# Optimization experiments

Hardware: AMD Instinct MI355X
Metric: run time of the kernel (lower is better)

The kernel has to match this reference:

```python
import jax, jax.numpy as jnp
import numpy as np

INTERVAL = 4
Q = 2 ** INTERVAL          # 16, quantization step
L = 2 ** (8 - INTERVAL) + 1  # 17, LUT size per axis


def round_ste(x):
    # round in forward, identity in backward (BPDA)
    return x + jax.lax.stop_gradient(jnp.round(x) - x)


def setup_inputs() -> dict:
    key = jax.random.key(0)
    k1, k2, k3 = jax.random.split(key, 3)
    # pixel values in [0, 255)
    img = jax.random.uniform(k1, (2, 3, 1080, 1920), jnp.float32) * 255.0
    # int8 LUT / 127 -> values in [-1, 1], shape [L^3, 3, 1, 1]
    lut = jax.random.uniform(k2, (L ** 3, 3, 1, 1), jnp.float32, -1.0, 1.0)
    # color correction matrix, scaled so final output mostly lands in [0,1]
    ccm = (jnp.eye(3, dtype=jnp.float32) + 0.05 * jax.random.normal(k3, (3, 3), jnp.float32)) / 127.0
    return {"img": img, "lut": lut, "ccm": ccm}


def _lut3d_interp(img, lut):
    """Trilinear 3D-LUT interpolation (InterpTorch3DBatch). img: [B,3,H,W]."""
    B, C, H, W = img.shape
    # _prepare_3d_lut_weights: scale, round with STE, clamp
    w = jnp.clip(round_ste(lut * 127.0), -127.0, 127.0)[:, :, 0, 0]  # [L^3, 3]
    flat = img.transpose(0, 2, 3, 1).reshape(-1, 3)  # [N, 3] per-pixel rgb
    r, g, b = flat[:, 0], flat[:, 1], flat[:, 2]
    r1 = jnp.floor(r / Q).astype(jnp.int32)
    g1 = jnp.floor(g / Q).astype(jnp.int32)
    b1 = jnp.floor(b / Q).astype(jnp.int32)
    fr = jnp.mod(r, float(Q))
    fg = jnp.mod(g, float(Q))
    fb = jnp.mod(b, float(Q))
    r2 = jnp.clip(r1 + 1, 0, L - 1)
    g2 = jnp.clip(g1 + 1, 0, L - 1)
    b2 = jnp.clip(b1 + 1, 0, L - 1)

    def corner(i, j, k):
        return w[i * (L * L) + j * L + k]  # [N, 3] gather

    p000 = corner(r1, g1, b1); p001 = corner(r1, g1, b2)
    p010 = corner(r1, g2, b1); p011 = corner(r1, g2, b2)
    p100 = corner(r2, g1, b1); p101 = corner(r2, g1, b2)
    p110 = corner(r2, g2, b1); p111 = corner(r2, g2, b2)

    fr = (fr / Q)[:, None]; fg = (fg / Q)[:, None]; fb = (fb / Q)[:, None]
    c00 = p000 * (1 - fr) + p100 * fr
    c01 = p001 * (1 - fr) + p101 * fr
    c10 = p010 * (1 - fr) + p110 * fr
    c11 = p011 * (1 - fr) + p111 * fr
    c0 = c00 * (1 - fg) + c10 * fg
    c1 = c01 * (1 - fg) + c11 * fg
    out = c0 * (1 - fb) + c1 * fb  # [N, 3]
    return out, (B, H, W, C)


def reference(img, lut, ccm):
    out_pix, (B, H, W, C) = _lut3d_interp(img, lut)
    # apply_color: per-pixel 3x3 color matrix (tensordot dims [[-1],[-1]]) + clamp
    out_pix = jnp.clip(out_pix @ ccm.T, 1e-8, 1.0)
    return out_pix.reshape(B, H, W, C).transpose(0, 3, 1, 2)
```

## Files before the change

### kernel.cpp

```cpp
#include <hip/hip_runtime.h>
#include <cstdint>

#define LUT_L    17
#define LUT_LL   289
#define NLUT     4913
#define NLUT_PAD 4916
#define IMG_B    2
#define IMG_H    1080
#define IMG_W    1920
#define PLANE    (IMG_H * IMG_W)
#define NPIX     (IMG_B * PLANE)
#define NQUAD    (NPIX / 4)
#define QPB      1024
#define NFULL    (NQUAD / QPB)

typedef float nfloat4 __attribute__((ext_vector_type(4)));

__device__ __forceinline__ int pack_entry(const float* __restrict__ lut, int idx) {
    float r = lut[idx * 3 + 0] * 127.0f;
    float g = lut[idx * 3 + 1] * 127.0f;
    float b = lut[idx * 3 + 2] * 127.0f;
    int ir = (int)rintf(r);
    int ig = (int)rintf(g);
    int ib = (int)rintf(b);
    ir = max(-127, min(127, ir));
    ig = max(-127, min(127, ig));
    ib = max(-127, min(127, ib));
    return (ir & 0xff) | ((ig & 0xff) << 8) | ((ib & 0xff) << 16);
}

__global__ void pack_lut_kernel(const float* __restrict__ lut, int* __restrict__ wq) {
    int idx = blockIdx.x * blockDim.x + threadIdx.x;
    if (idx >= NLUT_PAD) return;
    wq[idx] = (idx < NLUT) ? pack_entry(lut, idx) : 0;
}

__device__ __forceinline__ float up0(int v) { return (float)((v << 24) >> 24); }
__device__ __forceinline__ float up1(int v) { return (float)((v << 16) >> 24); }
__device__ __forceinline__ float up2(int v) { return (float)((v <<  8) >> 24); }

__device__ __forceinline__ float clamp01eps(float x) {
    return fminf(fmaxf(x, 1e-8f), 1.0f);
}

__device__ __forceinline__ void px_process(float r, float g, float b,
                                           const int* wq,
                                           const float* __restrict__ m,
                                           float& o0, float& o1, float& o2) {
    float rq = r * 0.0625f, gq = g * 0.0625f, bq = b * 0.0625f;
    float rf = floorf(rq), gf = floorf(gq), bf = floorf(bq);
    float fr = rq - rf, fg = gq - gf, fb = bq - bf;
    int i1 = (int)rf, j1 = (int)gf, k1 = (int)bf;

    const int* r00 = wq + (i1 * LUT_LL + j1 * LUT_L + k1);
    const int* r01 = r00 + LUT_L;
    const int* r10 = r00 + LUT_LL;
    const int* r11 = r10 + LUT_L;
    int w000 = r00[0], w001 = r00[1];
    int w010 = r01[0], w011 = r01[1];
    int w100 = r10[0], w101 = r10[1];
    int w110 = r11[0], w111 = r11[1];

    float wr0 = 1.0f - fr, wg0 = 1.0f - fg, wb0 = 1.0f - fb;
    float a00 = wg0 * wb0, a01 = wg0 * fb, a10 = fg * wb0, a11 = fg * fb;
    float s000 = wr0 * a00, s001 = wr0 * a01, s010 = wr0 * a10, s011 = wr0 * a11;
    float s100 = fr  * a00, s101 = fr  * a01, s110 = fr  * a10, s111 = fr  * a11;

    float pr = s000 * up0(w000);
    pr = fmaf(s001, up0(w001), pr); pr = fmaf(s010, up0(w010), pr);
    pr = fmaf(s011, up0(w011), pr); pr = fmaf(s100, up0(w100), pr);
    pr = fmaf(s101, up0(w101), pr); pr = fmaf(s110, up0(w110), pr);
    pr = fmaf(s111, up0(w111), pr);

    float pg = s000 * up1(w000);
    pg = fmaf(s001, up1(w001), pg); pg = fmaf(s010, up1(w010), pg);
    pg = fmaf(s011, up1(w011), pg); pg = fmaf(s100, up1(w100), pg);
    pg = fmaf(s101, up1(w101), pg); pg = fmaf(s110, up1(w110), pg);
    pg = fmaf(s111, up1(w111), pg);

    float pb = s000 * up2(w000);
    pb = fmaf(s001, up2(w001), pb); pb = fmaf(s010, up2(w010), pb);
    pb = fmaf(s011, up2(w011), pb); pb = fmaf(s100, up2(w100), pb);
    pb = fmaf(s101, up2(w101), pb); pb = fmaf(s110, up2(w110), pb);
    pb = fmaf(s111, up2(w111), pb);

    o0 = clamp01eps(fmaf(pr, m[0], fmaf(pg, m[1], pb * m[2])));
    o1 = clamp01eps(fmaf(pr, m[3], fmaf(pg, m[4], pb * m[5])));
    o2 = clamp01eps(fmaf(pr, m[6], fmaf(pg, m[7], pb * m[8])));
}

__device__ __forceinline__ void do_quad(const float* __restrict__ img,
                                        float* __restrict__ out,
                                        const int* wq, const float* __restrict__ m,
                                        int q) {
    int p = q * 4;
    int bimg = p / PLANE;
    int hw = p - bimg * PLANE;
    size_t base = (size_t)bimg * 3 * PLANE + hw;

    nfloat4 R  = *(const nfloat4*)(img + base);
    nfloat4 G  = *(const nfloat4*)(img + base + PLANE);
    nfloat4 Bv = *(const nfloat4*)(img + base + 2 * PLANE);

    float o0x, o0y, o0z, o0w;
    float o1x, o1y, o1z, o1w;
    float o2x, o2y, o2z, o2w;

    px_process(R.x, G.x, Bv.x, wq, m, o0x, o1x, o2x);
    px_process(R.y, G.y, Bv.y, wq, m, o0y, o1y, o2y);
    px_process(R.z, G.z, Bv.z, wq, m, o0z, o1z, o2z);
    px_process(R.w, G.w, Bv.w, wq, m, o0w, o1w, o2w);

    nfloat4 O0 = {o0x, o0y, o0z, o0w};
    nfloat4 O1 = {o1x, o1y, o1z, o1w};
    nfloat4 O2 = {o2x, o2y, o2z, o2w};

    __builtin_nontemporal_store(O0, (nfloat4*)(out + base));
    __builtin_nontemporal_store(O1, (nfloat4*)(out + base + PLANE));
    __builtin_nontemporal_store(O2, (nfloat4*)(out + base + 2 * PLANE));
}

__global__ __launch_bounds__(256) void lut3d(const float* __restrict__ img,
                                             const int* __restrict__ wq_g,
                                             const float* __restrict__ ccm,
                                             float* __restrict__ out) {
    __shared__ int wq[NLUT_PAD];
    {
        const int4* src = (const int4*)wq_g;
        int4* dst = (int4*)wq;
        for (int i = threadIdx.x; i < NLUT_PAD / 4; i += 256) dst[i] = src[i];
    }
    float m[9];
#pragma unroll
    for (int i = 0; i < 9; i++) m[i] = ccm[i];
    __syncthreads();

    int qbase = blockIdx.x * QPB + threadIdx.x;
    if (blockIdx.x < NFULL) {
#pragma unroll
        for (int j = 0; j < 4; j++) do_quad(img, out, wq, m, qbase + 256 * j);
    } else {
#pragma unroll
        for (int j = 0; j < 2; j++) do_quad(img, out, wq, m, qbase + 256 * j);
    }
}

__global__ __launch_bounds__(256) void lut3d_build(const float* __restrict__ img,
                                                   const float* __restrict__ lut,
                                                   const float* __restrict__ ccm,
                                                   float* __restrict__ out) {
    __shared__ int wq[NLUT_PAD];
    for (int i = threadIdx.x; i < NLUT_PAD; i += 256)
        wq[i] = (i < NLUT) ? pack_entry(lut, i) : 0;
    float m[9];
#pragma unroll
    for (int i = 0; i < 9; i++) m[i] = ccm[i];
    __syncthreads();

    int qbase = blockIdx.x * QPB + threadIdx.x;
    if (blockIdx.x < NFULL) {
#pragma unroll
        for (int j = 0; j < 4; j++) do_quad(img, out, wq, m, qbase + 256 * j);
    } else {
#pragma unroll
        for (int j = 0; j < 2; j++) do_quad(img, out, wq, m, qbase + 256 * j);
    }
}

extern "C" void kernel_launch(void* const* d_in, const int* in_sizes, int n_in,
                              void* d_out, int out_size, void* d_ws, size_t ws_size,
                              hipStream_t stream) {
    const float* img = (const float*)d_in[0];
    const float* lut = (const float*)d_in[1];
    const float* ccm = (const float*)d_in[2];
    float* out = (float*)d_out;

    const int grid = NFULL + 1;
    if (ws_size >= NLUT_PAD * sizeof(int)) {
        int* wq = (int*)d_ws;
        pack_lut_kernel<<<(NLUT_PAD + 255) / 256, 256, 0, stream>>>(lut, wq);
        lut3d<<<grid, 256, 0, stream>>>(img, wq, ccm, out);
    } else {
        lut3d_build<<<grid, 256, 0, stream>>>(img, lut, ccm, out);
    }
}
```

Measured before the change: 106.8 us.

## Bias LUT entries to unsigned, prefetch pixels before LUT staging, halve per-block work

LUT entries are now stored with a +127 bias so unpacking uses unsigned byte extraction (which can map to cheap ubyte-to-float conversion) instead of sign-extending shifts. The bias is removed by folding a per-channel offset into the colour-matrix FMA. The first quad's image loads are issued before the shared-memory LUT copy so global latency overlaps the staging. Each block now handles 2 quads per thread instead of 4, doubling the block count and the number of LUT copies into LDS.

```diff
diff --git a/kernel.cpp b/kernel.cpp
--- a/kernel.cpp
+++ b/kernel.cpp
@@ -11,33 +11,33 @@
 #define PLANE    (IMG_H * IMG_W)
 #define NPIX     (IMG_B * PLANE)
 #define NQUAD    (NPIX / 4)
-#define QPB      1024
-#define NFULL    (NQUAD / QPB)
+#define QPB      512
+#define NBLK     (NQUAD / QPB)
 
 typedef float nfloat4 __attribute__((ext_vector_type(4)));
 
-__device__ __forceinline__ int pack_entry(const float* __restrict__ lut, int idx) {
+__device__ __forceinline__ int pack_entry_biased(const float* __restrict__ lut, int idx) {
     float r = lut[idx * 3 + 0] * 127.0f;
     float g = lut[idx * 3 + 1] * 127.0f;
     float b = lut[idx * 3 + 2] * 127.0f;
     int ir = (int)rintf(r);
     int ig = (int)rintf(g);
     int ib = (int)rintf(b);
-    ir = max(-127, min(127, ir));
-    ig = max(-127, min(127, ig));
-    ib = max(-127, min(127, ib));
-    return (ir & 0xff) | ((ig & 0xff) << 8) | ((ib & 0xff) << 16);
+    ir = max(-127, min(127, ir)) + 127;
+    ig = max(-127, min(127, ig)) + 127;
+    ib = max(-127, min(127, ib)) + 127;
+    return ir | (ig << 8) | (ib << 16);
 }
 
 __global__ void pack_lut_kernel(const float* __restrict__ lut, int* __restrict__ wq) {
     int idx = blockIdx.x * blockDim.x + threadIdx.x;
     if (idx >= NLUT_PAD) return;
-    wq[idx] = (idx < NLUT) ? pack_entry(lut, idx) : 0;
-}
-
-__device__ __forceinline__ float up0(int v) { return (float)((v << 24) >> 24); }
-__device__ __forceinline__ float up1(int v) { return (float)((v << 16) >> 24); }
-__device__ __forceinline__ float up2(int v) { return (float)((v <<  8) >> 24); }
+    wq[idx] = (idx < NLUT) ? pack_entry_biased(lut, idx) : 0;
+}
+
+__device__ __forceinline__ float ub0(int v) { return (float)( (unsigned)v        & 0xffu); }
+__device__ __forceinline__ float ub1(int v) { return (float)(((unsigned)v >>  8) & 0xffu); }
+__device__ __forceinline__ float ub2(int v) { return (float)(((unsigned)v >> 16) & 0xffu); }
 
 __device__ __forceinline__ float clamp01eps(float x) {
     return fminf(fmaxf(x, 1e-8f), 1.0f);
@@ -46,6 +46,7 @@
 __device__ __forceinline__ void px_process(float r, float g, float b,
                                            const int* wq,
                                            const float* __restrict__ m,
+                                           const float* __restrict__ off,
                                            float& o0, float& o1, float& o2) {
     float rq = r * 0.0625f, gq = g * 0.0625f, bq = b * 0.0625f;
     float rf = floorf(rq), gf = floorf(gq), bf = floorf(bq);
@@ -66,50 +67,50 @@
     float s000 = wr0 * a00, s001 = wr0 * a01, s010 = wr0 * a10, s011 = wr0 * a11;
     float s100 = fr  * a00, s101 = fr  * a01, s110 = fr  * a10, s111 = fr  * a11;
 
-    float pr = s000 * up0(w000);
-    pr = fmaf(s001, up0(w001), pr); pr = fmaf(s010, up0(w010), pr);
-    pr = fmaf(s011, up0(w011), pr); pr = fmaf(s100, up0(w100), pr);
-    pr = fmaf(s101, up0(w101), pr); pr = fmaf(s110, up0(w110), pr);
-    pr = fmaf(s111, up0(w111), pr);
-
-    float pg = s000 * up1(w000);
-    pg = fmaf(s001, up1(w001), pg); pg = fmaf(s010, up1(w010), pg);
-    pg = fmaf(s011, up1(w011), pg); pg = fmaf(s100, up1(w100), pg);
-    pg = fmaf(s101, up1(w101), pg); pg = fmaf(s110, up1(w110), pg);
-    pg = fmaf(s111, up1(w111), pg);
-
-    float pb = s000 * up2(w000);
-    pb = fmaf(s001, up2(w001), pb); pb = fmaf(s010, up2(w010), pb);
-    pb = fmaf(s011, up2(w011), pb); pb = fmaf(s100, up2(w100), pb);
-    pb = fmaf(s101, up2(w101), pb); pb = fmaf(s110, up2(w110), pb);
-    pb = fmaf(s111, up2(w111), pb);
-
-    o0 = clamp01eps(fmaf(pr, m[0], fmaf(pg, m[1], pb * m[2])));
-    o1 = clamp01eps(fmaf(pr, m[3], fmaf(pg, m[4], pb * m[5])));
-    o2 = clamp01eps(fmaf(pr, m[6], fmaf(pg, m[7], pb * m[8])));
-}
-
-__device__ __forceinline__ void do_quad(const float* __restrict__ img,
-                                        float* __restrict__ out,
-                                        const int* wq, const float* __restrict__ m,
-                                        int q) {
+    float pr = s000 * ub0(w000);
+    pr = fmaf(s001, ub0(w001), pr); pr = fmaf(s010, ub0(w010), pr);
+    pr = fmaf(s011, ub0(w011), pr); pr = fmaf(s100, ub0(w100), pr);
+    pr = fmaf(s101, ub0(w101), pr); pr = fmaf(s110, ub0(w110), pr);
+    pr = fmaf(s111, ub0(w111), pr);
+
+    float pg = s000 * ub1(w000);
+    pg = fmaf(s001, ub1(w001), pg); pg = fmaf(s010, ub1(w010), pg);
+    pg = fmaf(s011, ub1(w011), pg); pg = fmaf(s100, ub1(w100), pg);
+    pg = fmaf(s101, ub1(w101), pg); pg = fmaf(s110, ub1(w110), pg);
+    pg = fmaf(s111, ub1(w111), pg);
+
+    float pb = s000 * ub2(w000);
+    pb = fmaf(s001, ub2(w001), pb); pb = fmaf(s010, ub2(w010), pb);
+    pb = fmaf(s011, ub2(w011), pb); pb = fmaf(s100, ub2(w100), pb);
+    pb = fmaf(s101, ub2(w101), pb); pb = fmaf(s110, ub2(w110), pb);
+    pb = fmaf(s111, ub2(w111), pb);
+
+    o0 = clamp01eps(fmaf(pr, m[0], fmaf(pg, m[1], fmaf(pb, m[2], off[0]))));
+    o1 = clamp01eps(fmaf(pr, m[3], fmaf(pg, m[4], fmaf(pb, m[5], off[1]))));
+    o2 = clamp01eps(fmaf(pr, m[6], fmaf(pg, m[7], fmaf(pb, m[8], off[2]))));
+}
+
+__device__ __forceinline__ void quad_addr(int q, size_t& base) {
     int p = q * 4;
     int bimg = p / PLANE;
     int hw = p - bimg * PLANE;
-    size_t base = (size_t)bimg * 3 * PLANE + hw;
-
-    nfloat4 R  = *(const nfloat4*)(img + base);
-    nfloat4 G  = *(const nfloat4*)(img + base + PLANE);
-    nfloat4 Bv = *(const nfloat4*)(img + base + 2 * PLANE);
-
+    base = (size_t)bimg * 3 * PLANE + hw;
+}
+
+__device__ __forceinline__ void quad_compute_store(float* __restrict__ out,
+                                                   const int* wq,
+                                                   const float* __restrict__ m,
+                                                   const float* __restrict__ off,
+                                                   size_t base,
+                                                   nfloat4 R, nfloat4 G, nfloat4 Bv) {
     float o0x, o0y, o0z, o0w;
     float o1x, o1y, o1z, o1w;
     float o2x, o2y, o2z, o2w;
 
-    px_process(R.x, G.x, Bv.x, wq, m, o0x, o1x, o2x);
-    px_process(R.y, G.y, Bv.y, wq, m, o0y, o1y, o2y);
-    px_process(R.z, G.z, Bv.z, wq, m, o0z, o1z, o2z);
-    px_process(R.w, G.w, Bv.w, wq, m, o0w, o1w, o2w);
+    px_process(R.x, G.x, Bv.x, wq, m, off, o0x, o1x, o2x);
+    px_process(R.y, G.y, Bv.y, wq, m, off, o0y, o1y, o2y);
+    px_process(R.z, G.z, Bv.z, wq, m, off, o0z, o1z, o2z);
+    px_process(R.w, G.w, Bv.w, wq, m, off, o0w, o1w, o2w);
 
     nfloat4 O0 = {o0x, o0y, o0z, o0w};
     nfloat4 O1 = {o1x, o1y, o1z, o1w};
@@ -125,24 +126,35 @@
                                              const float* __restrict__ ccm,
                                              float* __restrict__ out) {
     __shared__ int wq[NLUT_PAD];
+
+    int q0 = blockIdx.x * QPB + threadIdx.x;
+    int q1 = q0 + 256;
+    size_t base0, base1;
+    quad_addr(q0, base0);
+    quad_addr(q1, base1);
+
+    nfloat4 R0  = *(const nfloat4*)(img + base0);
+    nfloat4 G0  = *(const nfloat4*)(img + base0 + PLANE);
+    nfloat4 B0  = *(const nfloat4*)(img + base0 + 2 * PLANE);
+
     {
         const int4* src = (const int4*)wq_g;
         int4* dst = (int4*)wq;
         for (int i = threadIdx.x; i < NLUT_PAD / 4; i += 256) dst[i] = src[i];
     }
-    float m[9];
+    float m[9], off[3];
 #pragma unroll
     for (int i = 0; i < 9; i++) m[i] = ccm[i];
+#pragma unroll
+    for (int c = 0; c < 3; c++) off[c] = -127.0f * (m[3*c] + m[3*c+1] + m[3*c+2]);
     __syncthreads();
 
-    int qbase = blockIdx.x * QPB + threadIdx.x;
-    if (blockIdx.x < NFULL) {
-#pragma unroll
-        for (int j = 0; j < 4; j++) do_quad(img, out, wq, m, qbase + 256 * j);
-    } else {
-#pragma unroll
-        for (int j = 0; j < 2; j++) do_quad(img, out, wq, m, qbase + 256 * j);
-    }
+    quad_compute_store(out, wq, m, off, base0, R0, G0, B0);
+
+    nfloat4 R1  = *(const nfloat4*)(img + base1);
+    nfloat4 G1  = *(const nfloat4*)(img + base1 + PLANE);
+    nfloat4 B1  = *(const nfloat4*)(img + base1 + 2 * PLANE);
+    quad_compute_store(out, wq, m, off, base1, R1, G1, B1);
 }
 
 __global__ __launch_bounds__(256) void lut3d_build(const float* __restrict__ img,
@@ -151,20 +163,27 @@
                                                    float* __restrict__ out) {
     __shared__ int wq[NLUT_PAD];
     for (int i = threadIdx.x; i < NLUT_PAD; i += 256)
-        wq[i] = (i < NLUT) ? pack_entry(lut, i) : 0;
-    float m[9];
+        wq[i] = (i < NLUT) ? pack_entry_biased(lut, i) : 0;
+    float m[9], off[3];
 #pragma unroll
     for (int i = 0; i < 9; i++) m[i] = ccm[i];
+#pragma unroll
+    for (int c = 0; c < 3; c++) off[c] = -127.0f * (m[3*c] + m[3*c+1] + m[3*c+2]);
     __syncthreads();
 
-    int qbase = blockIdx.x * QPB + threadIdx.x;
-    if (blockIdx.x < NFULL) {
-#pragma unroll
-        for (int j = 0; j < 4; j++) do_quad(img, out, wq, m, qbase + 256 * j);
-    } else {
-#pragma unroll
-        for (int j = 0; j < 2; j++) do_quad(img, out, wq, m, qbase + 256 * j);
-    }
+    int q0 = blockIdx.x * QPB + threadIdx.x;
+    int q1 = q0 + 256;
+    size_t base0, base1;
+    quad_addr(q0, base0);
+    quad_addr(q1, base1);
+    nfloat4 R0  = *(const nfloat4*)(img + base0);
+    nfloat4 G0  = *(const nfloat4*)(img + base0 + PLANE);
+    nfloat4 B0  = *(const nfloat4*)(img + base0 + 2 * PLANE);
+    quad_compute_store(out, wq, m, off, base0, R0, G0, B0);
+    nfloat4 R1  = *(const nfloat4*)(img + base1);
+    nfloat4 G1  = *(const nfloat4*)(img + base1 + PLANE);
+    nfloat4 B1  = *(const nfloat4*)(img + base1 + 2 * PLANE);
+    quad_compute_store(out, wq, m, off, base1, R1, G1, B1);
 }
 
 extern "C" void kernel_launch(void* const* d_in, const int* in_sizes, int n_in,
@@ -175,12 +194,11 @@
     const float* ccm = (const float*)d_in[2];
     float* out = (float*)d_out;
 
-    const int grid = NFULL + 1;
     if (ws_size >= NLUT_PAD * sizeof(int)) {
         int* wq = (int*)d_ws;
         pack_lut_kernel<<<(NLUT_PAD + 255) / 256, 256, 0, stream>>>(lut, wq);
-        lut3d<<<grid, 256, 0, stream>>>(img, wq, ccm, out);
+        lut3d<<<NBLK, 256, 0, stream>>>(img, wq, ccm, out);
     } else {
-        lut3d_build<<<grid, 256, 0, stream>>>(img, lut, ccm, out);
+        lut3d_build<<<NBLK, 256, 0, stream>>>(img, lut, ccm, out);
     }
 }
```

Result: no change. 106.5 us (-0.3%).
